# Kernel tuning notes

Measured on AMD Instinct MI355X. Metric: run time of the kernel, lower is better.

The kernel has to match this reference:

```python
import jax, jax.numpy as jnp
import numpy as np

N = 100000      # num nodes
E = 1600000     # num edges
IN, HID, OUT = 256, 128, 64
ALPHA, BETA = 0.1, 1.0


def gcn_conv(x, W, b, src, dst, n):
    # PyG GCNConv: add self-loops, symmetric D^{-1/2}(A+I)D^{-1/2} normalization.
    h = x @ W  # [N, F]
    ones = jnp.ones((src.shape[0],), h.dtype)
    deg = jax.ops.segment_sum(ones, dst, num_segments=n) + 1.0  # +1 from self-loop
    dinv = jax.lax.rsqrt(deg)                                   # deg >= 1 always
    norm = dinv[src] * dinv[dst]                                # [E]
    out = jax.ops.segment_sum(norm[:, None] * h[src], dst, num_segments=n)
    out = out + (dinv * dinv)[:, None] * h                      # self-loop term
    return out + b


def group_softmax(v, seg, n):
    # torch_geometric.utils.softmax over dim 0 grouped by seg (max is detached in PyG).
    m = jax.ops.segment_max(v, seg, num_segments=n)
    num = jnp.exp(v - jax.lax.stop_gradient(m[seg]))
    den = jax.ops.segment_sum(num, seg, num_segments=n)
    return num / den[seg]


def reference(x, edge_index, edge_weight, W1, b1, W2, b2):
    src, dst = edge_index[0], edge_index[1]
    n = x.shape[0]
    h = jax.nn.relu(gcn_conv(x, W1, b1, src, dst, n))
    # F.dropout(training=False) in eval mode -> identity
    # crf_layer: per-edge scatter-add in both directions (vectorized segment_sum)
    w = (BETA * edge_weight)[:, None]  # [E,1]
    x_crf = (jax.ops.segment_sum(w * h[dst], src, num_segments=n)
             + jax.ops.segment_sum(w * h[src], dst, num_segments=n))
    # softmax(x_crf, arange(n)): each node is its own group (size 1) -> all ones.
    seg = jnp.arange(n)
    x_crf = group_softmax(x_crf, seg, n)
    h = (1.0 - ALPHA) * h + ALPHA * x_crf
    out = gcn_conv(h, W2, b2, src, dst, n)
    return jax.nn.log_softmax(out, axis=1)


def setup_inputs() -> dict:
    key = jax.random.key(0)
    k = jax.random.split(key, 6)
    x = jax.random.normal(k[0], (N, IN), jnp.float32)
    edge_index = jax.random.randint(k[1], (2, E), 0, N, dtype=jnp.int32)
    edge_weight = jnp.ones((E,), jnp.float32)
    W1 = jax.random.normal(k[2], (IN, HID), jnp.float32) * 0.05
    b1 = jnp.zeros((HID,), jnp.float32)
    W2 = jax.random.normal(k[3], (HID, OUT), jnp.float32) * 0.05
    b2 = jnp.zeros((OUT,), jnp.float32)
    return {"x": x, "edge_index": edge_index, "edge_weight": edge_weight,
            "W1": W1, "b1": b1, "W2": W2, "b2": b2}
```

## Files before the change

### kernel.cpp

```cpp
#include <hip/hip_runtime.h>
#include <math.h>


#define F_IN  256
#define F_HID 128
#define F_OUT 64
#define CSR_CAP 48
#define NBUCK 16
#define BSHIFT 13
#define BCAP  135000
#define BPAD  16

typedef __attribute__((ext_vector_type(8))) __bf16 bf16x8;
typedef __attribute__((ext_vector_type(8))) short  s16x8;
typedef __attribute__((ext_vector_type(4))) short  s16x4;
typedef __attribute__((ext_vector_type(4))) float  f32x4;

__device__ __forceinline__ unsigned short f2bf(float f) {
  unsigned u = __builtin_bit_cast(unsigned, f);
  u += 0x7fffu + ((u >> 16) & 1u);
  return (unsigned short)(u >> 16);
}
__device__ __forceinline__ float bf2f(unsigned short s) {
  unsigned u = ((unsigned)s) << 16;
  return __builtin_bit_cast(float, u);
}

__global__ void k_prep(const float* __restrict__ W1, const float* __restrict__ W2,
                       unsigned short* __restrict__ W1s, unsigned short* __restrict__ W2s,
                       int* __restrict__ zbase, int nzero) {
  const int i = blockIdx.x * 256 + threadIdx.x;
  if (i < nzero) zbase[i] = 0;
  if (i < 32768) {
    const int n = i >> 8, rem = i & 255;
    const int slot = rem >> 3, kb = rem & 7;
    const int k = ((slot ^ (n & 7)) << 3) | kb;
    W1s[i] = f2bf(W1[(size_t)k * F_HID + n]);
  } else if (i < 40960) {
    const int j = i - 32768;
    const int n = j >> 7, rem = j & 127;
    const int slot = rem >> 3, kb = rem & 7;
    const int k = ((slot ^ (n & 7)) << 3) | kb;
    W2s[j] = f2bf(W2[(size_t)k * F_OUT + n]);
  }
}

__global__ __launch_bounds__(256) void k_bin(const int* __restrict__ srcv,
                                             const int* __restrict__ dstv, int E,
                                             int* __restrict__ bcnt, uint2* __restrict__ bins) {
  __shared__ int lcnt[NBUCK];
  __shared__ int lbase[NBUCK];
  __shared__ int lpos[NBUCK];
  const int tid = threadIdx.x;
  const int per = (E + gridDim.x - 1) / gridDim.x;
  const int start = blockIdx.x * per;
  const int end = min(start + per, E);
  if (tid < NBUCK) lcnt[tid] = 0;
  __syncthreads();
  for (int e = start + tid; e < end; e += 256) {
    const int b = (int)((unsigned)dstv[e] >> BSHIFT);
    atomicAdd(&lcnt[b], 1);
  }
  __syncthreads();
  if (tid < NBUCK) {
    lbase[tid] = atomicAdd(&bcnt[tid * BPAD], lcnt[tid]);
    lpos[tid] = 0;
  }
  __syncthreads();
  for (int e = start + tid; e < end; e += 256) {
    uint2 p;
    p.x = (unsigned)srcv[e];
    p.y = (unsigned)dstv[e];
    const int b = (int)(p.y >> BSHIFT);
    const int pos = lbase[b] + atomicAdd(&lpos[b], 1);
    if (pos < BCAP) bins[(size_t)b * BCAP + pos] = p;
  }
}

__global__ __launch_bounds__(256) void k_fill_b(const uint2* __restrict__ bins,
                                                const int* __restrict__ bcnt,
                                                int* __restrict__ cnt, int* __restrict__ csr) {
  const int bucket = blockIdx.x & 15;
  const int slice = blockIdx.x >> 4;
  const int nsl = gridDim.x >> 4;
  int c = bcnt[bucket * BPAD];
  if (c > BCAP) c = BCAP;
  const uint2* bp = bins + (size_t)bucket * BCAP;
  for (int i = slice * 256 + threadIdx.x; i < c; i += nsl * 256) {
    const uint2 p = bp[i];
    const int pos = atomicAdd(&cnt[p.y], 1);
    if (pos < CSR_CAP) csr[(size_t)p.y * CSR_CAP + pos] = (int)p.x;
  }
}

__global__ void k_dinv(const int* __restrict__ cnt, float* __restrict__ dinv, int N) {
  int i = blockIdx.x * blockDim.x + threadIdx.x;
  if (i < N) dinv[i] = rsqrtf((float)cnt[i] + 1.0f);
}

__global__ __launch_bounds__(256) void k_gemm1(const float* __restrict__ X,
                                               const unsigned short* __restrict__ W1s,
                                               unsigned short* __restrict__ H, int M) {
  __shared__ unsigned short Bs[128][256];
  const int tid = threadIdx.x;
  {
    const s16x8* src = (const s16x8*)W1s;
    s16x8* dst = (s16x8*)&Bs[0][0];
#pragma unroll
    for (int i = 0; i < 16; ++i) dst[i * 256 + tid] = src[i * 256 + tid];
  }
  const int lane = tid & 63;
  const int wv_ = tid >> 6;
  const int l15 = lane & 15;
  const int kgrp = (lane >> 4) << 3;
  const int rowA = blockIdx.x * 64 + wv_ * 16 + l15;
  const int rA = rowA < M ? rowA : M - 1;
  const float* xp = &X[(size_t)rA * F_IN + kgrp];

  f32x4 acc[8];
#pragma unroll
  for (int i = 0; i < 8; ++i) acc[i] = (f32x4){0.f, 0.f, 0.f, 0.f};

  float4 a0 = *(const float4*)(xp);
  float4 a1 = *(const float4*)(xp + 4);
  __syncthreads();

#pragma unroll
  for (int k0 = 0; k0 < F_IN; k0 += 32) {
    bf16x8 af;
    {
      const float av[8] = {a0.x, a0.y, a0.z, a0.w, a1.x, a1.y, a1.z, a1.w};
#pragma unroll
      for (int j = 0; j < 8; ++j) af[j] = (__bf16)av[j];
    }
    if (k0 + 32 < F_IN) {
      a0 = *(const float4*)(xp + k0 + 32);
      a1 = *(const float4*)(xp + k0 + 36);
    }
    const int kc = (k0 + kgrp) >> 3;
#pragma unroll
    for (int nf = 0; nf < 8; ++nf) {
      const int n = nf * 16 + l15;
      const s16x8 braw = *(const s16x8*)&Bs[n][(kc ^ (n & 7)) << 3];
      const bf16x8 bv = __builtin_bit_cast(bf16x8, braw);
      acc[nf] = __builtin_amdgcn_mfma_f32_16x16x32_bf16(af, bv, acc[nf], 0, 0, 0);
    }
  }
  const int rowD = blockIdx.x * 64 + wv_ * 16 + ((lane >> 4) << 2);
#pragma unroll
  for (int r = 0; r < 4; ++r) {
    if (rowD + r < M) {
      unsigned short* hp = &H[(size_t)(rowD + r) * F_HID + l15];
#pragma unroll
      for (int nf = 0; nf < 8; ++nf) hp[nf * 16] = f2bf(acc[nf][r]);
    }
  }
}

__global__ __launch_bounds__(256) void k_gemm2(const unsigned short* __restrict__ A1,
                                               const unsigned short* __restrict__ W2s,
                                               unsigned short* __restrict__ H2, int M) {
  __shared__ unsigned short Bs[64][128];
  const int tid = threadIdx.x;
  {
    const s16x8* src = (const s16x8*)W2s;
    s16x8* dst = (s16x8*)&Bs[0][0];
#pragma unroll
    for (int i = 0; i < 4; ++i) dst[i * 256 + tid] = src[i * 256 + tid];
  }
  const int lane = tid & 63;
  const int wv_ = tid >> 6;
  const int l15 = lane & 15;
  const int kgrp = (lane >> 4) << 3;
  const int rowA = blockIdx.x * 64 + wv_ * 16 + l15;
  const int rA = rowA < M ? rowA : M - 1;
  const unsigned short* ap = &A1[(size_t)rA * F_HID + kgrp];

  f32x4 acc[4];
#pragma unroll
  for (int i = 0; i < 4; ++i) acc[i] = (f32x4){0.f, 0.f, 0.f, 0.f};

  s16x8 raw = *(const s16x8*)(ap);
  __syncthreads();

#pragma unroll
  for (int k0 = 0; k0 < F_HID; k0 += 32) {
    bf16x8 af;
#pragma unroll
    for (int j = 0; j < 8; ++j) {
      float f = bf2f((unsigned short)raw[j]);
      f = 0.9f * fmaxf(f, 0.0f) + 0.1f;
      af[j] = (__bf16)f;
    }
    if (k0 + 32 < F_HID) raw = *(const s16x8*)(ap + k0 + 32);
    const int kc = (k0 + kgrp) >> 3;
#pragma unroll
    for (int nf = 0; nf < 4; ++nf) {
      const int n = nf * 16 + l15;
      const s16x8 braw = *(const s16x8*)&Bs[n][(kc ^ (n & 7)) << 3];
      const bf16x8 bv = __builtin_bit_cast(bf16x8, braw);
      acc[nf] = __builtin_amdgcn_mfma_f32_16x16x32_bf16(af, bv, acc[nf], 0, 0, 0);
    }
  }
  const int rowD = blockIdx.x * 64 + wv_ * 16 + ((lane >> 4) << 2);
#pragma unroll
  for (int r = 0; r < 4; ++r) {
    if (rowD + r < M) {
      unsigned short* hp = &H2[(size_t)(rowD + r) * F_OUT + l15];
#pragma unroll
      for (int nf = 0; nf < 4; ++nf) hp[nf * 16] = f2bf(acc[nf][r]);
    }
  }
}

__global__ __launch_bounds__(256) void k_gather1(const int* __restrict__ cnt,
                                                 const int* __restrict__ csr,
                                                 const float* __restrict__ dinv,
                                                 const unsigned short* __restrict__ h0,
                                                 const float* __restrict__ b1,
                                                 unsigned short* __restrict__ agg1, int N) {
  const int node = (blockIdx.x << 2) + (threadIdx.x >> 6);
  if (node >= N) return;
  const int lane = threadIdx.x & 63;
  const int grp = lane >> 4;
  const int l15 = lane & 15;
  int d_ = cnt[node];
  if (d_ > CSR_CAP) d_ = CSR_CAP;
  const float dv = dinv[node];
  int mysrc = 0;
  float myw = 0.f;
  if (lane < d_) {
    mysrc = csr[(size_t)node * CSR_CAP + lane];
    myw = dinv[mysrc] * dv;
  }
  float acc[8] = {0.f, 0.f, 0.f, 0.f, 0.f, 0.f, 0.f, 0.f};
  const int nq = (d_ + 3) >> 2;
#pragma unroll 2
  for (int q = 0; q < nq; ++q) {
    const int idx = (q << 2) + grp;
    const int s = __shfl(mysrc, idx);
    const float w = __shfl(myw, idx);
    const s16x8 v = *(const s16x8*)&h0[(size_t)s * F_HID + l15 * 8];
#pragma unroll
    for (int i = 0; i < 8; ++i) acc[i] += w * bf2f((unsigned short)v[i]);
  }
#pragma unroll
  for (int i = 0; i < 8; ++i) {
    acc[i] += __shfl_xor(acc[i], 16);
    acc[i] += __shfl_xor(acc[i], 32);
  }
  if (grp == 0) {
    const s16x8 sv = *(const s16x8*)&h0[(size_t)node * F_HID + l15 * 8];
    const float4 bb0 = *(const float4*)&b1[l15 * 8];
    const float4 bb1 = *(const float4*)&b1[l15 * 8 + 4];
    const float bl[8] = {bb0.x, bb0.y, bb0.z, bb0.w, bb1.x, bb1.y, bb1.z, bb1.w};
    const float d2 = dv * dv;
    s16x8 o;
#pragma unroll
    for (int i = 0; i < 8; ++i)
      o[i] = (short)f2bf(acc[i] + d2 * bf2f((unsigned short)sv[i]) + bl[i]);
    *(s16x8*)&agg1[(size_t)node * F_HID + l15 * 8] = o;
  }
}

__global__ __launch_bounds__(256) void k_gather2_lsm(const int* __restrict__ cnt,
                                                     const int* __restrict__ csr,
                                                     const float* __restrict__ dinv,
                                                     const unsigned short* __restrict__ h2,
                                                     const float* __restrict__ b2,
                                                     float* __restrict__ outv, int N) {
  const int node = (blockIdx.x << 2) + (threadIdx.x >> 6);
  if (node >= N) return;
  const int lane = threadIdx.x & 63;
  const int grp = lane >> 4;
  const int l15 = lane & 15;
  int d_ = cnt[node];
  if (d_ > CSR_CAP) d_ = CSR_CAP;
  const float dv = dinv[node];
  int mysrc = 0;
  float myw = 0.f;
  if (lane < d_) {
    mysrc = csr[(size_t)node * CSR_CAP + lane];
    myw = dinv[mysrc] * dv;
  }
  float acc[4] = {0.f, 0.f, 0.f, 0.f};
  const int nq = (d_ + 3) >> 2;
#pragma unroll 2
  for (int q = 0; q < nq; ++q) {
    const int idx = (q << 2) + grp;
    const int s = __shfl(mysrc, idx);
    const float w = __shfl(myw, idx);
    const s16x4 v = *(const s16x4*)&h2[(size_t)s * F_OUT + l15 * 4];
#pragma unroll
    for (int i = 0; i < 4; ++i) acc[i] += w * bf2f((unsigned short)v[i]);
  }
#pragma unroll
  for (int i = 0; i < 4; ++i) {
    acc[i] += __shfl_xor(acc[i], 16);
    acc[i] += __shfl_xor(acc[i], 32);
  }
  const s16x4 sv = *(const s16x4*)&h2[(size_t)node * F_OUT + l15 * 4];
  const float4 bb = *(const float4*)&b2[l15 * 4];
  const float bl[4] = {bb.x, bb.y, bb.z, bb.w};
  const float d2 = dv * dv;
  float lg[4];
#pragma unroll
  for (int i = 0; i < 4; ++i) lg[i] = acc[i] + d2 * bf2f((unsigned short)sv[i]) + bl[i];
  float m = fmaxf(fmaxf(lg[0], lg[1]), fmaxf(lg[2], lg[3]));
#pragma unroll
  for (int off = 1; off < 16; off <<= 1) m = fmaxf(m, __shfl_xor(m, off));
  float s = 0.f;
#pragma unroll
  for (int i = 0; i < 4; ++i) s += expf(lg[i] - m);
#pragma unroll
  for (int off = 1; off < 16; off <<= 1) s += __shfl_xor(s, off);
  const float lse = m + logf(s);
  if (grp == 0) {
    float4 o = {lg[0] - lse, lg[1] - lse, lg[2] - lse, lg[3] - lse};
    *(float4*)&outv[(size_t)node * F_OUT + l15 * 4] = o;
  }
}

extern "C" void kernel_launch(void* const* d_in, const int* in_sizes, int n_in,
                              void* d_out, int out_size, void* d_ws, size_t ws_size,
                              hipStream_t stream) {
  const float* x  = (const float*)d_in[0];
  const int*   ei = (const int*)d_in[1];
  const float* W1 = (const float*)d_in[3];
  const float* b1 = (const float*)d_in[4];
  const float* W2 = (const float*)d_in[5];
  const float* b2 = (const float*)d_in[6];

  const int N = in_sizes[0] / F_IN;
  const int E = in_sizes[1] / 2;
  const int* srcv = ei;
  const int* dstv = ei + E;

  float* ws = (float*)d_ws;
  const size_t Na = ((size_t)N + 511) & ~(size_t)255;
  int* bcnt = (int*)ws;
  int* cnt  = bcnt + NBUCK * BPAD;
  float* dinv = ws + Na;
  unsigned short* W1s = (unsigned short*)(ws + 2 * Na);
  unsigned short* W2s = (unsigned short*)(ws + 2 * Na + 16384);
  int* csr = (int*)(ws + 2 * Na + 16384 + 4096);
  size_t off = 2 * Na + 16384 + 4096 + (((size_t)N * CSR_CAP + 255) & ~(size_t)255);
  unsigned short* h2b   = (unsigned short*)(ws + off);
  off += ((size_t)N * (F_OUT / 2) + 255) & ~(size_t)255;
  unsigned short* agg1b = (unsigned short*)(ws + off);
  off += ((size_t)N * (F_HID / 2) + 255) & ~(size_t)255;
  unsigned short* h0b   = (unsigned short*)(ws + off);
  uint2* bins = (uint2*)h0b;
  float* outp = (float*)d_out;

  const int nzero = N + NBUCK * BPAD;
  const int prep_grid = (max(nzero, 40960) + 255) / 256;
  k_prep<<<prep_grid, 256, 0, stream>>>(W1, W2, W1s, W2s, bcnt, nzero);
  k_bin<<<512, 256, 0, stream>>>(srcv, dstv, E, bcnt, bins);
  k_fill_b<<<1024, 256, 0, stream>>>(bins, bcnt, cnt, csr);
  k_dinv<<<(N + 255) / 256, 256, 0, stream>>>(cnt, dinv, N);

  k_gemm1<<<(N + 63) / 64, 256, 0, stream>>>(x, W1s, h0b, N);
  k_gather1<<<(N + 3) / 4, 256, 0, stream>>>(cnt, csr, dinv, h0b, b1, agg1b, N);

  k_gemm2<<<(N + 63) / 64, 256, 0, stream>>>(agg1b, W2s, h2b, N);
  k_gather2_lsm<<<(N + 3) / 4, 256, 0, stream>>>(cnt, csr, dinv, h2b, b2, outp, N);
}
```

Before: 427.7 us.

## Store GEMM outputs as FP8 and recompute degree normalization inline

The intermediate feature matrices h0 and h2 are now stored as FP8 instead of bf16, which halves the bytes read by the two gather kernels. The gathers are re-laid out so 8 neighbors are processed per step with 8 lanes per row. The separate dinv kernel and buffer are removed, and rsqrt of the degree is computed on the fly from cnt. This cuts memory traffic in the bandwidth-bound gathers, at the cost of much lower precision in the aggregated features, which may exceed the accuracy tolerance. The bins buffer no longer aliases h0, so workspace use grows.

```diff
diff --git a/kernel.cpp b/kernel.cpp
--- a/kernel.cpp
+++ b/kernel.cpp
@@ -13,17 +13,16 @@
 
 typedef __attribute__((ext_vector_type(8))) __bf16 bf16x8;
 typedef __attribute__((ext_vector_type(8))) short  s16x8;
-typedef __attribute__((ext_vector_type(4))) short  s16x4;
 typedef __attribute__((ext_vector_type(4))) float  f32x4;
+typedef __attribute__((ext_vector_type(2))) float  f32x2;
 
 __device__ __forceinline__ unsigned short f2bf(float f) {
   unsigned u = __builtin_bit_cast(unsigned, f);
   u += 0x7fffu + ((u >> 16) & 1u);
   return (unsigned short)(u >> 16);
 }
-__device__ __forceinline__ float bf2f(unsigned short s) {
-  unsigned u = ((unsigned)s) << 16;
-  return __builtin_bit_cast(float, u);
+__device__ __forceinline__ unsigned char f2fp8(float f) {
+  return (unsigned char)(__builtin_amdgcn_cvt_pk_fp8_f32(f, f, 0, false) & 0xff);
 }
 
 __global__ void k_prep(const float* __restrict__ W1, const float* __restrict__ W2,
@@ -93,14 +92,9 @@
   }
 }
 
-__global__ void k_dinv(const int* __restrict__ cnt, float* __restrict__ dinv, int N) {
-  int i = blockIdx.x * blockDim.x + threadIdx.x;
-  if (i < N) dinv[i] = rsqrtf((float)cnt[i] + 1.0f);
-}
-
 __global__ __launch_bounds__(256) void k_gemm1(const float* __restrict__ X,
                                                const unsigned short* __restrict__ W1s,
-                                               unsigned short* __restrict__ H, int M) {
+                                               unsigned char* __restrict__ Hq, int M) {
   __shared__ unsigned short Bs[128][256];
   const int tid = threadIdx.x;
   {
@@ -150,16 +144,16 @@
 #pragma unroll
   for (int r = 0; r < 4; ++r) {
     if (rowD + r < M) {
-      unsigned short* hp = &H[(size_t)(rowD + r) * F_HID + l15];
-#pragma unroll
-      for (int nf = 0; nf < 8; ++nf) hp[nf * 16] = f2bf(acc[nf][r]);
+      unsigned char* hp = &Hq[(size_t)(rowD + r) * F_HID + l15];
+#pragma unroll
+      for (int nf = 0; nf < 8; ++nf) hp[nf * 16] = f2fp8(acc[nf][r]);
     }
   }
 }
 
 __global__ __launch_bounds__(256) void k_gemm2(const unsigned short* __restrict__ A1,
                                                const unsigned short* __restrict__ W2s,
-                                               unsigned short* __restrict__ H2, int M) {
+                                               unsigned char* __restrict__ H2q, int M) {
   __shared__ unsigned short Bs[64][128];
   const int tid = threadIdx.x;
   {
@@ -188,7 +182,8 @@
     bf16x8 af;
 #pragma unroll
     for (int j = 0; j < 8; ++j) {
-      float f = bf2f((unsigned short)raw[j]);
+      unsigned u = ((unsigned)(unsigned short)raw[j]) << 16;
+      float f = __builtin_bit_cast(float, u);
       f = 0.9f * fmaxf(f, 0.0f) + 0.1f;
       af[j] = (__bf16)f;
     }
@@ -206,118 +201,154 @@
 #pragma unroll
   for (int r = 0; r < 4; ++r) {
     if (rowD + r < M) {
-      unsigned short* hp = &H2[(size_t)(rowD + r) * F_OUT + l15];
-#pragma unroll
-      for (int nf = 0; nf < 4; ++nf) hp[nf * 16] = f2bf(acc[nf][r]);
+      unsigned char* hp = &H2q[(size_t)(rowD + r) * F_OUT + l15];
+#pragma unroll
+      for (int nf = 0; nf < 4; ++nf) hp[nf * 16] = f2fp8(acc[nf][r]);
     }
   }
 }
 
 __global__ __launch_bounds__(256) void k_gather1(const int* __restrict__ cnt,
                                                  const int* __restrict__ csr,
-                                                 const float* __restrict__ dinv,
-                                                 const unsigned short* __restrict__ h0,
+                                                 const unsigned char* __restrict__ h0q,
                                                  const float* __restrict__ b1,
                                                  unsigned short* __restrict__ agg1, int N) {
   const int node = (blockIdx.x << 2) + (threadIdx.x >> 6);
   if (node >= N) return;
   const int lane = threadIdx.x & 63;
-  const int grp = lane >> 4;
-  const int l15 = lane & 15;
+  const int grp = lane >> 3;
+  const int l7 = lane & 7;
   int d_ = cnt[node];
   if (d_ > CSR_CAP) d_ = CSR_CAP;
-  const float dv = dinv[node];
+  const float dv = rsqrtf((float)cnt[node] + 1.0f);
   int mysrc = 0;
   float myw = 0.f;
   if (lane < d_) {
     mysrc = csr[(size_t)node * CSR_CAP + lane];
-    myw = dinv[mysrc] * dv;
-  }
-  float acc[8] = {0.f, 0.f, 0.f, 0.f, 0.f, 0.f, 0.f, 0.f};
-  const int nq = (d_ + 3) >> 2;
+    myw = rsqrtf((float)cnt[mysrc] + 1.0f) * dv;
+  }
+  float acc[16] = {0.f, 0.f, 0.f, 0.f, 0.f, 0.f, 0.f, 0.f,
+                   0.f, 0.f, 0.f, 0.f, 0.f, 0.f, 0.f, 0.f};
+  const int nq = (d_ + 7) >> 3;
 #pragma unroll 2
   for (int q = 0; q < nq; ++q) {
-    const int idx = (q << 2) + grp;
+    const int idx = (q << 3) + grp;
     const int s = __shfl(mysrc, idx);
     const float w = __shfl(myw, idx);
-    const s16x8 v = *(const s16x8*)&h0[(size_t)s * F_HID + l15 * 8];
-#pragma unroll
-    for (int i = 0; i < 8; ++i) acc[i] += w * bf2f((unsigned short)v[i]);
-  }
-#pragma unroll
-  for (int i = 0; i < 8; ++i) {
+    const uint4 v = *(const uint4*)&h0q[(size_t)s * F_HID + l7 * 16];
+    const unsigned vv[4] = {v.x, v.y, v.z, v.w};
+#pragma unroll
+    for (int c = 0; c < 4; ++c) {
+      const f32x2 p0 = __builtin_amdgcn_cvt_pk_f32_fp8((int)vv[c], false);
+      const f32x2 p1 = __builtin_amdgcn_cvt_pk_f32_fp8((int)vv[c], true);
+      acc[c * 4 + 0] += w * p0[0];
+      acc[c * 4 + 1] += w * p0[1];
+      acc[c * 4 + 2] += w * p1[0];
+      acc[c * 4 + 3] += w * p1[1];
+    }
+  }
+#pragma unroll
+  for (int i = 0; i < 16; ++i) {
+    acc[i] += __shfl_xor(acc[i], 8);
     acc[i] += __shfl_xor(acc[i], 16);
     acc[i] += __shfl_xor(acc[i], 32);
   }
   if (grp == 0) {
-    const s16x8 sv = *(const s16x8*)&h0[(size_t)node * F_HID + l15 * 8];
-    const float4 bb0 = *(const float4*)&b1[l15 * 8];
-    const float4 bb1 = *(const float4*)&b1[l15 * 8 + 4];
-    const float bl[8] = {bb0.x, bb0.y, bb0.z, bb0.w, bb1.x, bb1.y, bb1.z, bb1.w};
+    const uint4 sv = *(const uint4*)&h0q[(size_t)node * F_HID + l7 * 16];
+    const unsigned svv[4] = {sv.x, sv.y, sv.z, sv.w};
+    float svf[16];
+#pragma unroll
+    for (int c = 0; c < 4; ++c) {
+      const f32x2 p0 = __builtin_amdgcn_cvt_pk_f32_fp8((int)svv[c], false);
+      const f32x2 p1 = __builtin_amdgcn_cvt_pk_f32_fp8((int)svv[c], true);
+      svf[c * 4 + 0] = p0[0]; svf[c * 4 + 1] = p0[1];
+      svf[c * 4 + 2] = p1[0]; svf[c * 4 + 3] = p1[1];
+    }
     const float d2 = dv * dv;
-    s16x8 o;
-#pragma unroll
-    for (int i = 0; i < 8; ++i)
-      o[i] = (short)f2bf(acc[i] + d2 * bf2f((unsigned short)sv[i]) + bl[i]);
-    *(s16x8*)&agg1[(size_t)node * F_HID + l15 * 8] = o;
+    s16x8 o0, o1;
+#pragma unroll
+    for (int i = 0; i < 8; ++i) {
+      const float b = b1[l7 * 16 + i];
+      o0[i] = (short)f2bf(acc[i] + d2 * svf[i] + b);
+    }
+#pragma unroll
+    for (int i = 0; i < 8; ++i) {
+      const float b = b1[l7 * 16 + 8 + i];
+      o1[i] = (short)f2bf(acc[8 + i] + d2 * svf[8 + i] + b);
+    }
+    *(s16x8*)&agg1[(size_t)node * F_HID + l7 * 16] = o0;
+    *(s16x8*)&agg1[(size_t)node * F_HID + l7 * 16 + 8] = o1;
   }
 }
 
 __global__ __launch_bounds__(256) void k_gather2_lsm(const int* __restrict__ cnt,
                                                      const int* __restrict__ csr,
-                                                     const float* __restrict__ dinv,
-                                                     const unsigned short* __restrict__ h2,
+                                                     const unsigned char* __restrict__ h2q,
                                                      const float* __restrict__ b2,
                                                      float* __restrict__ outv, int N) {
   const int node = (blockIdx.x << 2) + (threadIdx.x >> 6);
   if (node >= N) return;
   const int lane = threadIdx.x & 63;
-  const int grp = lane >> 4;
-  const int l15 = lane & 15;
+  const int grp = lane >> 3;
+  const int l7 = lane & 7;
   int d_ = cnt[node];
   if (d_ > CSR_CAP) d_ = CSR_CAP;
-  const float dv = dinv[node];
+  const float dv = rsqrtf((float)cnt[node] + 1.0f);
   int mysrc = 0;
   float myw = 0.f;
   if (lane < d_) {
     mysrc = csr[(size_t)node * CSR_CAP + lane];
-    myw = dinv[mysrc] * dv;
-  }
-  float acc[4] = {0.f, 0.f, 0.f, 0.f};
-  const int nq = (d_ + 3) >> 2;
+    myw = rsqrtf((float)cnt[mysrc] + 1.0f) * dv;
+  }
+  float acc[8] = {0.f, 0.f, 0.f, 0.f, 0.f, 0.f, 0.f, 0.f};
+  const int nq = (d_ + 7) >> 3;
 #pragma unroll 2
   for (int q = 0; q < nq; ++q) {
-    const int idx = (q << 2) + grp;
+    const int idx = (q << 3) + grp;
     const int s = __shfl(mysrc, idx);
     const float w = __shfl(myw, idx);
-    const s16x4 v = *(const s16x4*)&h2[(size_t)s * F_OUT + l15 * 4];
-#pragma unroll
-    for (int i = 0; i < 4; ++i) acc[i] += w * bf2f((unsigned short)v[i]);
-  }
-#pragma unroll
-  for (int i = 0; i < 4; ++i) {
+    const uint2 v = *(const uint2*)&h2q[(size_t)s * F_OUT + l7 * 8];
+    const f32x2 p0 = __builtin_amdgcn_cvt_pk_f32_fp8((int)v.x, false);
+    const f32x2 p1 = __builtin_amdgcn_cvt_pk_f32_fp8((int)v.x, true);
+    const f32x2 p2 = __builtin_amdgcn_cvt_pk_f32_fp8((int)v.y, false);
+    const f32x2 p3 = __builtin_amdgcn_cvt_pk_f32_fp8((int)v.y, true);
+    acc[0] += w * p0[0]; acc[1] += w * p0[1];
+    acc[2] += w * p1[0]; acc[3] += w * p1[1];
+    acc[4] += w * p2[0]; acc[5] += w * p2[1];
+    acc[6] += w * p3[0]; acc[7] += w * p3[1];
+  }
+#pragma unroll
+  for (int i = 0; i < 8; ++i) {
+    acc[i] += __shfl_xor(acc[i], 8);
     acc[i] += __shfl_xor(acc[i], 16);
     acc[i] += __shfl_xor(acc[i], 32);
   }
-  const s16x4 sv = *(const s16x4*)&h2[(size_t)node * F_OUT + l15 * 4];
-  const float4 bb = *(const float4*)&b2[l15 * 4];
-  const float bl[4] = {bb.x, bb.y, bb.z, bb.w};
+  const uint2 sv = *(const uint2*)&h2q[(size_t)node * F_OUT + l7 * 8];
+  const f32x2 q0 = __builtin_amdgcn_cvt_pk_f32_fp8((int)sv.x, false);
+  const f32x2 q1 = __builtin_amdgcn_cvt_pk_f32_fp8((int)sv.x, true);
+  const f32x2 q2 = __builtin_amdgcn_cvt_pk_f32_fp8((int)sv.y, false);
+  const f32x2 q3 = __builtin_amdgcn_cvt_pk_f32_fp8((int)sv.y, true);
+  const float svf[8] = {q0[0], q0[1], q1[0], q1[1], q2[0], q2[1], q3[0], q3[1]};
   const float d2 = dv * dv;
-  float lg[4];
-#pragma unroll
-  for (int i = 0; i < 4; ++i) lg[i] = acc[i] + d2 * bf2f((unsigned short)sv[i]) + bl[i];
-  float m = fmaxf(fmaxf(lg[0], lg[1]), fmaxf(lg[2], lg[3]));
-#pragma unroll
-  for (int off = 1; off < 16; off <<= 1) m = fmaxf(m, __shfl_xor(m, off));
+  float lg[8];
+#pragma unroll
+  for (int i = 0; i < 8; ++i) lg[i] = acc[i] + d2 * svf[i] + b2[l7 * 8 + i];
+  float m = lg[0];
+#pragma unroll
+  for (int i = 1; i < 8; ++i) m = fmaxf(m, lg[i]);
+#pragma unroll
+  for (int off = 1; off < 8; off <<= 1) m = fmaxf(m, __shfl_xor(m, off));
   float s = 0.f;
 #pragma unroll
-  for (int i = 0; i < 4; ++i) s += expf(lg[i] - m);
-#pragma unroll
-  for (int off = 1; off < 16; off <<= 1) s += __shfl_xor(s, off);
+  for (int i = 0; i < 8; ++i) s += expf(lg[i] - m);
+#pragma unroll
+  for (int off = 1; off < 8; off <<= 1) s += __shfl_xor(s, off);
   const float lse = m + logf(s);
   if (grp == 0) {
-    float4 o = {lg[0] - lse, lg[1] - lse, lg[2] - lse, lg[3] - lse};
-    *(float4*)&outv[(size_t)node * F_OUT + l15 * 4] = o;
+    float4 o0 = {lg[0] - lse, lg[1] - lse, lg[2] - lse, lg[3] - lse};
+    float4 o1 = {lg[4] - lse, lg[5] - lse, lg[6] - lse, lg[7] - lse};
+    *(float4*)&outv[(size_t)node * F_OUT + l7 * 8] = o0;
+    *(float4*)&outv[(size_t)node * F_OUT + l7 * 8 + 4] = o1;
   }
 }
 
@@ -340,17 +371,17 @@
   const size_t Na = ((size_t)N + 511) & ~(size_t)255;
   int* bcnt = (int*)ws;
   int* cnt  = bcnt + NBUCK * BPAD;
-  float* dinv = ws + Na;
-  unsigned short* W1s = (unsigned short*)(ws + 2 * Na);
-  unsigned short* W2s = (unsigned short*)(ws + 2 * Na + 16384);
-  int* csr = (int*)(ws + 2 * Na + 16384 + 4096);
-  size_t off = 2 * Na + 16384 + 4096 + (((size_t)N * CSR_CAP + 255) & ~(size_t)255);
-  unsigned short* h2b   = (unsigned short*)(ws + off);
-  off += ((size_t)N * (F_OUT / 2) + 255) & ~(size_t)255;
+  unsigned short* W1s = (unsigned short*)(ws + Na);
+  unsigned short* W2s = (unsigned short*)(ws + Na + 16384);
+  int* csr = (int*)(ws + Na + 16384 + 4096);
+  size_t off = Na + 16384 + 4096 + (((size_t)N * CSR_CAP + 255) & ~(size_t)255);
+  unsigned char* h2q = (unsigned char*)(ws + off);
+  off += (((size_t)N * 16) + 255) & ~(size_t)255;
   unsigned short* agg1b = (unsigned short*)(ws + off);
-  off += ((size_t)N * (F_HID / 2) + 255) & ~(size_t)255;
-  unsigned short* h0b   = (unsigned short*)(ws + off);
-  uint2* bins = (uint2*)h0b;
+  off += (((size_t)N * 64) + 255) & ~(size_t)255;
+  unsigned char* h0q = (unsigned char*)(ws + off);
+  off += (((size_t)N * 32) + 255) & ~(size_t)255;
+  uint2* bins = (uint2*)(ws + off);
   float* outp = (float*)d_out;
 
   const int nzero = N + NBUCK * BPAD;
@@ -358,11 +389,10 @@
   k_prep<<<prep_grid, 256, 0, stream>>>(W1, W2, W1s, W2s, bcnt, nzero);
   k_bin<<<512, 256, 0, stream>>>(srcv, dstv, E, bcnt, bins);
   k_fill_b<<<1024, 256, 0, stream>>>(bins, bcnt, cnt, csr);
-  k_dinv<<<(N + 255) / 256, 256, 0, stream>>>(cnt, dinv, N);
-
-  k_gemm1<<<(N + 63) / 64, 256, 0, stream>>>(x, W1s, h0b, N);
-  k_gather1<<<(N + 3) / 4, 256, 0, stream>>>(cnt, csr, dinv, h0b, b1, agg1b, N);
-
-  k_gemm2<<<(N + 63) / 64, 256, 0, stream>>>(agg1b, W2s, h2b, N);
-  k_gather2_lsm<<<(N + 3) / 4, 256, 0, stream>>>(cnt, csr, dinv, h2b, b2, outp, N);
-}
+
+  k_gemm1<<<(N + 63) / 64, 256, 0, stream>>>(x, W1s, h0q, N);
+  k_gather1<<<(N + 3) / 4, 256, 0, stream>>>(cnt, csr, h0q, b1, agg1b, N);
+
+  k_gemm2<<<(N + 63) / 64, 256, 0, stream>>>(agg1b, W2s, h2q, N);
+  k_gather2_lsm<<<(N + 3) / 4, 256, 0, stream>>>(cnt, csr, h2q, b2, outp, N);
+}
```

Measured after the change: 422.2 us. No clear change (-1.3%).
